# Performance work log

Measured on AMD Instinct MI355X. Metric: run time of the kernel, lower is better.

The kernel has to match this reference:

```python
import jax, jax.numpy as jnp
import numpy as np

EPS = 1e-5

def _fake_quant(w, axis):
    # symmetric int8 fake-quant with straight-through estimator
    s = jnp.max(jnp.abs(w), axis=axis, keepdims=True) / 127.0 + 1e-8
    q = jnp.clip(jnp.round(w / s), -127.0, 127.0) * s
    return w + jax.lax.stop_gradient(q - w)

def _qconv1x1(x, w, b):
    # x: [B, C_in, Q, H, W]; w: [C_out, C_in] (1x1 kernel); weight fake-quantized
    wq = _fake_quant(w, axis=1)
    return jnp.einsum('bcqhw,oc->boqhw', x, wq) + b[None, :, None, None, None]

def setup_inputs() -> dict:
    key = jax.random.key(0)
    ks = jax.random.split(key, 12)
    B, C, Q, H, W = 8, 256, 4, 40, 40
    x = jax.random.normal(ks[0], (B, C, Q, H, W), dtype=jnp.float32)
    scale = 1.0 / np.sqrt(C)
    Wq = jax.random.normal(ks[1], (C, C), dtype=jnp.float32) * scale
    Wk = jax.random.normal(ks[2], (C, C), dtype=jnp.float32) * scale
    Wv = jax.random.normal(ks[3], (C, C), dtype=jnp.float32) * scale
    Wp = jax.random.normal(ks[4], (C, C), dtype=jnp.float32) * scale
    bq = jnp.zeros((C,), jnp.float32)
    bk = jnp.zeros((C,), jnp.float32)
    bv = jnp.zeros((C,), jnp.float32)
    bp = jnp.zeros((C,), jnp.float32)
    gamma = jnp.ones((C,), jnp.float32)
    beta = jnp.zeros((C,), jnp.float32)
    return {"x": x, "Wq": Wq, "bq": bq, "Wk": Wk, "bk": bk,
            "Wv": Wv, "bv": bv, "Wp": Wp, "bp": bp,
            "gamma": gamma, "beta": beta}

def reference(x, Wq, bq, Wk, bk, Wv, bv, Wp, bp, gamma, beta):
    B, C, Q, H, W = x.shape
    q = _qconv1x1(x, Wq, bq)
    k = _qconv1x1(x, Wk, bk)
    v = _qconv1x1(x, Wv, bv)
    # per-rotation channel attention: [B, Q=4, C, H*W]
    qh = q.reshape(B, C, Q, H * W).transpose(0, 2, 1, 3)
    kh = k.reshape(B, C, Q, H * W).transpose(0, 2, 1, 3)
    vh = v.reshape(B, C, Q, H * W).transpose(0, 2, 1, 3)
    scale = 1.0 / jnp.sqrt(jnp.float32(C // 4))
    attn = jnp.einsum('bqcn,bqdn->bqcd', qh, kh) * scale  # [B,4,C,C]
    attn = jax.nn.softmax(attn, axis=-1)
    out = jnp.einsum('bqcd,bqdn->bqcn', attn, vh)  # [B,4,C,HW]
    out = out.transpose(0, 2, 1, 3).reshape(B, C, Q, H, W)
    out = _qconv1x1(out, Wp, bp)
    # IQBN: per-channel batchnorm with int8 fake-quantized gamma
    mean = jnp.mean(out, axis=(0, 2, 3, 4), keepdims=True)
    var = jnp.var(out, axis=(0, 2, 3, 4), keepdims=True)
    g = _fake_quant(gamma, axis=None)[None, :, None, None, None]
    b = beta[None, :, None, None, None]
    out = (out - mean) * jax.lax.rsqrt(var + EPS) * g + b
    return out
```

## Files before the change

kernel.cpp:

```cpp
#include <hip/hip_runtime.h>
#include <math.h>

#define BB 8
#define CCH 256
#define QQ 4
#define NN 1600
#define BQN 32
#define SP 51200
#define EPSF 1e-5f

typedef __attribute__((ext_vector_type(8))) short bf16x8;
typedef __attribute__((ext_vector_type(4))) float f32x4;

static __device__ inline ushort f2bf(float f) {
  union { float f; unsigned u; } v; v.f = f;
  return (ushort)((v.u + 0x7fffu + ((v.u >> 16) & 1u)) >> 16);
}
static __device__ inline float bf2f(ushort u) {
  union { unsigned u; float f; } v; v.u = ((unsigned)u) << 16;
  return v.f;
}
static __device__ inline void gld16(const ushort* g, ushort* l) {
  __builtin_amdgcn_global_load_lds(
      (const __attribute__((address_space(1))) unsigned int*)g,
      (__attribute__((address_space(3))) unsigned int*)l, 16, 0, 0);
}

__global__ void quant_weights_kernel(const float* Wq, const float* Wk,
                                     const float* Wv, const float* Wp,
                                     const float* gamma,
                                     ushort* wq, ushort* wk, ushort* wvT, ushort* wp,
                                     float* gq, float* r) {
  __shared__ float red[256];
  int blk = blockIdx.x;
  int tid = threadIdx.x;
  if (blk < 1024) {
    int mat = blk >> 8;
    int row = blk & 255;
    const float* W = (mat == 0) ? Wq : (mat == 1) ? Wk : (mat == 2) ? Wv : Wp;
    float w = W[row * 256 + tid];
    red[tid] = fabsf(w);
    __syncthreads();
    for (int s = 128; s > 0; s >>= 1) {
      if (tid < s) red[tid] = fmaxf(red[tid], red[tid + s]);
      __syncthreads();
    }
    float s = red[0] / 127.0f + 1e-8f;
    float q = fminf(fmaxf(rintf(w / s), -127.0f), 127.0f) * s;
    ushort qb = f2bf(q);
    if (mat == 0)      wq[row * 256 + tid] = qb;
    else if (mat == 1) wk[row * 256 + tid] = qb;
    else if (mat == 2) wvT[tid * 256 + row] = qb;
    else               wp[row * 256 + tid] = qb;
  } else {
    float g = gamma[tid];
    red[tid] = fabsf(g);
    __syncthreads();
    for (int s = 128; s > 0; s >>= 1) {
      if (tid < s) red[tid] = fmaxf(red[tid], red[tid + s]);
      __syncthreads();
    }
    float s = red[0] / 127.0f + 1e-8f;
    gq[tid] = fminf(fmaxf(rintf(g / s), -127.0f), 127.0f) * s;
    for (int i = tid; i < BQN * 256; i += 256) r[i] = 0.f;
  }
}

__global__ __launch_bounds__(256)
void prep_kernel(const float* __restrict__ x, ushort* __restrict__ xb,
                 ushort* __restrict__ xT, float* __restrict__ r) {
  int bqi = blockIdx.z, b = bqi >> 2, q = bqi & 3;
  int s0 = blockIdx.x * 64, c0 = blockIdx.y * 64;
  __shared__ ushort lT[64 * 66];
  int tid = threadIdx.x;
  int c = tid >> 2, nch = (tid & 3) * 16;
  const float* xp = x + ((size_t)(b * CCH + c0 + c) * QQ + q) * NN + s0 + nch;
  union { ushort u[16]; int4 v[2]; } nb;
  float s = 0.f;
#pragma unroll
  for (int j = 0; j < 4; j++) {
    float4 f = ((const float4*)xp)[j];
    s += f.x + f.y + f.z + f.w;
    nb.u[j * 4 + 0] = f2bf(f.x);
    nb.u[j * 4 + 1] = f2bf(f.y);
    nb.u[j * 4 + 2] = f2bf(f.z);
    nb.u[j * 4 + 3] = f2bf(f.w);
    lT[c * 66 + nch + j * 4 + 0] = nb.u[j * 4 + 0];
    lT[c * 66 + nch + j * 4 + 1] = nb.u[j * 4 + 1];
    lT[c * 66 + nch + j * 4 + 2] = nb.u[j * 4 + 2];
    lT[c * 66 + nch + j * 4 + 3] = nb.u[j * 4 + 3];
  }
  ushort* xbp = xb + (size_t)bqi * (CCH * NN) + (size_t)(c0 + c) * NN + s0 + nch;
  *(int4*)xbp = nb.v[0];
  *((int4*)xbp + 1) = nb.v[1];
  s += __shfl_down(s, 2);
  s += __shfl_down(s, 1);
  if ((tid & 3) == 0) atomicAdd(&r[bqi * 256 + c0 + c], s);
  __syncthreads();
  int n = tid >> 2, cch = (tid & 3) * 16;
  union { ushort u[16]; int4 v[2]; } o;
#pragma unroll
  for (int i = 0; i < 16; i++) o.u[i] = lT[(cch + i) * 66 + n];
  ushort* dst = xT + (size_t)(bqi * NN + s0 + n) * CCH + c0 + cch;
  *(int4*)dst = o.v[0];
  *((int4*)dst + 1) = o.v[1];
}

__global__ __launch_bounds__(256)
void gram_kernel(const ushort* __restrict__ xb, ushort* __restrict__ Gh,
                 ushort* __restrict__ Gl) {
  __shared__ __align__(16) char smem[32768];
  float* lC = (float*)smem;
  int z = blockIdx.z;
  int mBase = blockIdx.y * 128, nBase = blockIdx.x * 128;
  int tid = threadIdx.x, wave = tid >> 6, lane = tid & 63;
  int wm = wave >> 1, wn = wave & 1;
  int col = lane & 15, quad = lane >> 4;
  int srow = tid >> 2, skc = (tid & 3) * 8;
  const ushort* X = xb + (size_t)z * (CCH * NN);
  const ushort* gA  = X + (size_t)(mBase + srow) * NN + skc;
  const ushort* gA2 = gA + (size_t)64 * NN;
  const ushort* gB  = X + (size_t)(nBase + srow) * NN + skc;
  const ushort* gB2 = gB + (size_t)64 * NN;
  ushort* sA1[2]; ushort* sA2[2]; ushort* sB1[2]; ushort* sB2[2];
#pragma unroll
  for (int b = 0; b < 2; b++) {
    ushort* lAb = (ushort*)(smem + b * 16384);
    ushort* lBb = (ushort*)(smem + b * 16384 + 8192);
    sA1[b] = &lAb[srow * 32 + skc];
    sA2[b] = &lAb[(64 + srow) * 32 + skc];
    sB1[b] = &lBb[srow * 32 + skc];
    sB2[b] = &lBb[(64 + srow) * 32 + skc];
  }
  f32x4 acc[4][4];
#pragma unroll
  for (int i = 0; i < 4; i++)
#pragma unroll
    for (int j = 0; j < 4; j++) acc[i][j] = (f32x4){0.f, 0.f, 0.f, 0.f};

  const int nIter = NN / 32;
  gld16(gA, sA1[0]); gld16(gA2, sA2[0]); gld16(gB, sB1[0]); gld16(gB2, sB2[0]);
  for (int it = 0; it < nIter; ++it) {
    int cur = it & 1;
    __syncthreads();
    if (it + 1 < nIter) {
      int kt = (it + 1) << 5, nxt = cur ^ 1;
      gld16(gA + kt, sA1[nxt]); gld16(gA2 + kt, sA2[nxt]);
      gld16(gB + kt, sB1[nxt]); gld16(gB2 + kt, sB2[nxt]);
    }
    const ushort* lAc = (const ushort*)(smem + cur * 16384);
    const ushort* lBc = (const ushort*)(smem + cur * 16384 + 8192);
    bf16x8 af[4], bfr[4];
#pragma unroll
    for (int i = 0; i < 4; i++)
      af[i] = *(const bf16x8*)&lAc[(wm * 64 + i * 16 + col) * 32 + quad * 8];
#pragma unroll
    for (int j = 0; j < 4; j++)
      bfr[j] = *(const bf16x8*)&lBc[(wn * 64 + j * 16 + col) * 32 + quad * 8];
#pragma unroll
    for (int i = 0; i < 4; i++)
#pragma unroll
      for (int j = 0; j < 4; j++)
        acc[i][j] = __builtin_amdgcn_mfma_f32_16x16x32_bf16(af[i], bfr[j], acc[i][j], 0, 0, 0);
  }
  __syncthreads();
  float* lCw = lC + wave * 16 * 68;
  int mW = mBase + wm * 64, nW = nBase + wn * 64;
#pragma unroll
  for (int i = 0; i < 4; i++) {
#pragma unroll
    for (int j = 0; j < 4; j++)
#pragma unroll
      for (int rg = 0; rg < 4; rg++)
        lCw[(quad * 4 + rg) * 68 + j * 16 + col] = acc[i][j][rg];
    int mrow0 = mW + i * 16;
    int rr = lane & 15, cc = lane >> 4;
    union { ushort u[16]; int4 v[2]; } oh, ol;
#pragma unroll
    for (int t = 0; t < 16; t++) {
      float vfl = lCw[rr * 68 + cc * 16 + t];
      ushort hh = f2bf(vfl);
      oh.u[t] = hh;
      ol.u[t] = f2bf(vfl - bf2f(hh));
    }
    size_t off = (size_t)z * 65536 + (size_t)(mrow0 + rr) * 256 + nW + cc * 16;
    *(int4*)(Gh + off) = oh.v[0];
    *((int4*)(Gh + off) + 1) = oh.v[1];
    *(int4*)(Gl + off) = ol.v[0];
    *((int4*)(Gl + off) + 1) = ol.v[1];
  }
}

template<int MODE>
__global__ __launch_bounds__(256)
void gemm256(const ushort* __restrict__ A, long sA, const ushort* __restrict__ A2,
             const ushort* __restrict__ B, long sB, const ushort* __restrict__ B2,
             void* __restrict__ C1, void* __restrict__ C2, long sC) {
  __shared__ __align__(16) char smem[24576];
  ushort* lA = (ushort*)smem;
  ushort* lB = (ushort*)(smem + 8192);
  ushort* lX = (ushort*)(smem + 16384);
  float* lC = (float*)smem;
  int z = blockIdx.z;
  int mBase = blockIdx.y * 128, nBase = blockIdx.x * 128;
  int tid = threadIdx.x, wave = tid >> 6, lane = tid & 63;
  int wm = wave >> 1, wn = wave & 1;
  int col = lane & 15, quad = lane >> 4;
  int srow = tid >> 2, skc = (tid & 3) * 8;
  const ushort* Az = A + (size_t)z * sA;
  const ushort* Bz = B + (size_t)z * sB;
  const ushort* gA  = Az + (size_t)(mBase + srow) * 256 + skc;
  const ushort* gA2r = gA + 64 * 256;
  const ushort* gB  = Bz + (size_t)(nBase + srow) * 256 + skc;
  const ushort* gB2r = gB + 64 * 256;
  const ushort* gX = nullptr;
  const ushort* gX2 = nullptr;
  if (MODE == 0) {
    const ushort* Xz = B2 + (size_t)z * sB;
    gX = Xz + (size_t)(nBase + srow) * 256 + skc;
    gX2 = gX + 64 * 256;
  } else if (MODE == 1) {
    const ushort* Xz = A2 + (size_t)z * sA;
    gX = Xz + (size_t)(mBase + srow) * 256 + skc;
    gX2 = gX + 64 * 256;
  }
  ushort* dA1 = &lA[srow * 32 + skc]; ushort* dA2 = &lA[(64 + srow) * 32 + skc];
  ushort* dB1 = &lB[srow * 32 + skc]; ushort* dB2 = &lB[(64 + srow) * 32 + skc];
  ushort* dX1 = &lX[srow * 32 + skc]; ushort* dX2 = &lX[(64 + srow) * 32 + skc];

  f32x4 acc[4][4];
#pragma unroll
  for (int i = 0; i < 4; i++)
#pragma unroll
    for (int j = 0; j < 4; j++) acc[i][j] = (f32x4){0.f, 0.f, 0.f, 0.f};

  for (int kt = 0; kt < 256; kt += 32) {
    __syncthreads();
    gld16(gA + kt, dA1); gld16(gA2r + kt, dA2);
    gld16(gB + kt, dB1); gld16(gB2r + kt, dB2);
    if (MODE <= 1) { gld16(gX + kt, dX1); gld16(gX2 + kt, dX2); }
    __syncthreads();
    bf16x8 af[4], bfr[4], xf[4];
#pragma unroll
    for (int i = 0; i < 4; i++)
      af[i] = *(const bf16x8*)&lA[(wm * 64 + i * 16 + col) * 32 + quad * 8];
#pragma unroll
    for (int j = 0; j < 4; j++)
      bfr[j] = *(const bf16x8*)&lB[(wn * 64 + j * 16 + col) * 32 + quad * 8];
    if (MODE == 0) {
#pragma unroll
      for (int j = 0; j < 4; j++)
        xf[j] = *(const bf16x8*)&lX[(wn * 64 + j * 16 + col) * 32 + quad * 8];
    } else if (MODE == 1) {
#pragma unroll
      for (int i = 0; i < 4; i++)
        xf[i] = *(const bf16x8*)&lX[(wm * 64 + i * 16 + col) * 32 + quad * 8];
    }
#pragma unroll
    for (int i = 0; i < 4; i++)
#pragma unroll
      for (int j = 0; j < 4; j++) {
        acc[i][j] = __builtin_amdgcn_mfma_f32_16x16x32_bf16(af[i], bfr[j], acc[i][j], 0, 0, 0);
        if (MODE == 0)
          acc[i][j] = __builtin_amdgcn_mfma_f32_16x16x32_bf16(af[i], xf[j], acc[i][j], 0, 0, 0);
        else if (MODE == 1)
          acc[i][j] = __builtin_amdgcn_mfma_f32_16x16x32_bf16(xf[i], bfr[j], acc[i][j], 0, 0, 0);
      }
  }
  __syncthreads();
  float* lCw = lC + wave * 16 * 68;
  int mW = mBase + wm * 64, nW = nBase + wn * 64;
#pragma unroll
  for (int i = 0; i < 4; i++) {
#pragma unroll
    for (int j = 0; j < 4; j++)
#pragma unroll
      for (int rg = 0; rg < 4; rg++)
        lCw[(quad * 4 + rg) * 68 + j * 16 + col] = acc[i][j][rg];
    int mrow0 = mW + i * 16;
    int rr = lane & 15, cc = lane >> 4;
    if (MODE == 0) {
      union { ushort u[16]; int4 v[2]; } oh, ol;
#pragma unroll
      for (int t = 0; t < 16; t++) {
        float vfl = lCw[rr * 68 + cc * 16 + t];
        ushort hh = f2bf(vfl);
        oh.u[t] = hh;
        ol.u[t] = f2bf(vfl - bf2f(hh));
      }
      size_t off = (size_t)z * sC + (size_t)(mrow0 + rr) * 256 + nW + cc * 16;
      *(int4*)((ushort*)C1 + off) = oh.v[0];
      *((int4*)((ushort*)C1 + off) + 1) = oh.v[1];
      *(int4*)((ushort*)C2 + off) = ol.v[0];
      *((int4*)((ushort*)C2 + off) + 1) = ol.v[1];
    } else if (MODE == 1) {
      float* C = (float*)C1 + (size_t)z * sC + (size_t)(mrow0 + rr) * 256 + nW + cc * 16;
#pragma unroll
      for (int v = 0; v < 4; v++) {
        float4 f;
        f.x = lCw[rr * 68 + cc * 16 + v * 4 + 0];
        f.y = lCw[rr * 68 + cc * 16 + v * 4 + 1];
        f.z = lCw[rr * 68 + cc * 16 + v * 4 + 2];
        f.w = lCw[rr * 68 + cc * 16 + v * 4 + 3];
        *(float4*)(C + v * 4) = f;
      }
    } else if (MODE == 2) {
      int n = nW + lane;
      union { ushort u[16]; int4 v[2]; } o;
#pragma unroll
      for (int t = 0; t < 16; t++) o.u[t] = f2bf(lCw[t * 68 + lane]);
      ushort* C = (ushort*)C1 + (size_t)z * sC + (size_t)n * 256 + mrow0;
      *(int4*)C = o.v[0];
      *((int4*)C + 1) = o.v[1];
    } else {
      union { ushort u[16]; int4 v[2]; } o;
#pragma unroll
      for (int t = 0; t < 16; t++) o.u[t] = f2bf(lCw[rr * 68 + cc * 16 + t]);
      ushort* C = (ushort*)C1 + (size_t)z * sC + (size_t)(mrow0 + rr) * 256 + nW + cc * 16;
      *(int4*)C = o.v[0];
      *((int4*)C + 1) = o.v[1];
    }
  }
}

__global__ void uv_kernel(const ushort* __restrict__ wq, const ushort* __restrict__ wk,
                          const float* __restrict__ r, float* __restrict__ u,
                          float* __restrict__ vv) {
  int bq = blockIdx.x, sel = blockIdx.y, c = threadIdx.x;
  const ushort* W = sel ? wk : wq;
  float s = 0.f;
  for (int i = 0; i < 256; i++) s += bf2f(W[c * 256 + i]) * r[bq * 256 + i];
  (sel ? vv : u)[bq * 256 + c] = s;
}

__global__ void softmax_kernel(const float* __restrict__ S, const float* __restrict__ u,
                               const float* __restrict__ vv, const float* __restrict__ bqv,
                               const float* __restrict__ bkv, const float* __restrict__ bvv,
                               ushort* __restrict__ P, float* __restrict__ pb) {
  int bi = blockIdx.x;
  int bq = bi >> 8, rw = bi & 255;
  int tid = threadIdx.x;
  size_t off = (size_t)bq * 65536 + (size_t)rw * 256 + tid;
  float bqc = bqv[rw], bkd = bkv[tid];
  float val = 0.125f * (S[off] + u[bq * 256 + rw] * bkd + bqc * vv[bq * 256 + tid]
                        + 1600.0f * bqc * bkd);
  __shared__ float red[256];
  red[tid] = val;
  __syncthreads();
  for (int s = 128; s > 0; s >>= 1) {
    if (tid < s) red[tid] = fmaxf(red[tid], red[tid + s]);
    __syncthreads();
  }
  float m = red[0];
  __syncthreads();
  float e = expf(val - m);
  red[tid] = e;
  __syncthreads();
  for (int s = 128; s > 0; s >>= 1) {
    if (tid < s) red[tid] += red[tid + s];
    __syncthreads();
  }
  float p = e / red[0];
  P[off] = f2bf(p);
  __syncthreads();
  red[tid] = p * bvv[tid];
  __syncthreads();
  for (int s = 128; s > 0; s >>= 1) {
    if (tid < s) red[tid] += red[tid + s];
    __syncthreads();
  }
  if (tid == 0) pb[bq * 256 + rw] = red[0];
}

__global__ void bo_kernel(const ushort* __restrict__ wp, const float* __restrict__ pb,
                          const float* __restrict__ bp, float* __restrict__ bo) {
  int bq = blockIdx.x, o = threadIdx.x;
  float s = bp[o];
  for (int c = 0; c < 256; c++) s += bf2f(wp[o * 256 + c]) * pb[bq * 256 + c];
  bo[bq * 256 + o] = s;
}

__global__ __launch_bounds__(256)
void final_kernel(const ushort* __restrict__ Tm, const ushort* __restrict__ xT,
                  const float* __restrict__ bo, float* __restrict__ out,
                  float* __restrict__ part) {
  __shared__ __align__(16) char smem[32768];
  float* lC = (float*)smem;
  __shared__ float psS[2][128];
  __shared__ float psS2[2][128];
  int z = blockIdx.z;
  int mBase = blockIdx.y * 128, nBase = blockIdx.x * 128;
  int tid = threadIdx.x, wave = tid >> 6, lane = tid & 63;
  int wm = wave >> 1, wn = wave & 1;
  int col = lane & 15, quad = lane >> 4;
  int srow = tid >> 2, skc = (tid & 3) * 8;
  const ushort* Az = Tm + (size_t)z * 65536;
  const ushort* Bz = xT + (size_t)z * (NN * 256);
  const ushort* gA  = Az + (size_t)(mBase + srow) * 256 + skc;
  const ushort* gA2 = gA + 64 * 256;
  int br1 = nBase + srow;      br1 = br1 < NN ? br1 : NN - 1;
  int br2 = nBase + 64 + srow; br2 = br2 < NN ? br2 : NN - 1;
  const ushort* gB  = Bz + (size_t)br1 * 256 + skc;
  const ushort* gB2 = Bz + (size_t)br2 * 256 + skc;
  ushort* sA1[2]; ushort* sA2[2]; ushort* sB1[2]; ushort* sB2[2];
#pragma unroll
  for (int b = 0; b < 2; b++) {
    ushort* lAb = (ushort*)(smem + b * 16384);
    ushort* lBb = (ushort*)(smem + b * 16384 + 8192);
    sA1[b] = &lAb[srow * 32 + skc];
    sA2[b] = &lAb[(64 + srow) * 32 + skc];
    sB1[b] = &lBb[srow * 32 + skc];
    sB2[b] = &lBb[(64 + srow) * 32 + skc];
  }
  f32x4 acc[4][4];
#pragma unroll
  for (int i = 0; i < 4; i++)
#pragma unroll
    for (int j = 0; j < 4; j++) acc[i][j] = (f32x4){0.f, 0.f, 0.f, 0.f};

  const int nIter = 8;
  gld16(gA, sA1[0]); gld16(gA2, sA2[0]); gld16(gB, sB1[0]); gld16(gB2, sB2[0]);
  for (int it = 0; it < nIter; ++it) {
    int cur = it & 1;
    __syncthreads();
    if (it + 1 < nIter) {
      int kt = (it + 1) << 5, nxt = cur ^ 1;
      gld16(gA + kt, sA1[nxt]); gld16(gA2 + kt, sA2[nxt]);
      gld16(gB + kt, sB1[nxt]); gld16(gB2 + kt, sB2[nxt]);
    }
    const ushort* lAc = (const ushort*)(smem + cur * 16384);
    const ushort* lBc = (const ushort*)(smem + cur * 16384 + 8192);
    bf16x8 af[4], bfr[4];
#pragma unroll
    for (int i = 0; i < 4; i++)
      af[i] = *(const bf16x8*)&lAc[(wm * 64 + i * 16 + col) * 32 + quad * 8];
#pragma unroll
    for (int j = 0; j < 4; j++)
      bfr[j] = *(const bf16x8*)&lBc[(wn * 64 + j * 16 + col) * 32 + quad * 8];
#pragma unroll
    for (int i = 0; i < 4; i++)
#pragma unroll
      for (int j = 0; j < 4; j++)
        acc[i][j] = __builtin_amdgcn_mfma_f32_16x16x32_bf16(af[i], bfr[j], acc[i][j], 0, 0, 0);
  }
  __syncthreads();
  float* lCw = lC + wave * 16 * 68;
  int mW = mBase + wm * 64, nW = nBase + wn * 64;
  int b = z >> 2, q = z & 3;
#pragma unroll
  for (int i = 0; i < 4; i++) {
#pragma unroll
    for (int j = 0; j < 4; j++)
#pragma unroll
      for (int rg = 0; rg < 4; rg++)
        lCw[(quad * 4 + rg) * 68 + j * 16 + col] = acc[i][j][rg];
    int mrow0 = mW + i * 16;
    int rr = lane & 15, cc = lane >> 4;
    int n0 = nW + cc * 16;
    float bi = bo[(size_t)z * 256 + mrow0 + rr];
    float ls = 0.f, ls2 = 0.f;
    if (n0 < NN) {
      float* C = out + (size_t)b * (CCH * QQ * NN)
               + (size_t)(mrow0 + rr) * (QQ * NN) + (size_t)q * NN + n0;
#pragma unroll
      for (int v = 0; v < 4; v++) {
        float4 f;
        f.x = lCw[rr * 68 + cc * 16 + v * 4 + 0] + bi;
        f.y = lCw[rr * 68 + cc * 16 + v * 4 + 1] + bi;
        f.z = lCw[rr * 68 + cc * 16 + v * 4 + 2] + bi;
        f.w = lCw[rr * 68 + cc * 16 + v * 4 + 3] + bi;
        *(float4*)(C + v * 4) = f;
        ls  += f.x + f.y + f.z + f.w;
        ls2 += f.x * f.x + f.y * f.y + f.z * f.z + f.w * f.w;
      }
    }
    ls  += __shfl_down(ls, 32);  ls  += __shfl_down(ls, 16);
    ls2 += __shfl_down(ls2, 32); ls2 += __shfl_down(ls2, 16);
    if (lane < 16) {
      psS[wn][wm * 64 + i * 16 + lane] = ls;
      psS2[wn][wm * 64 + i * 16 + lane] = ls2;
    }
  }
  __syncthreads();
  if (tid < 128) {
    float s  = psS[0][tid] + psS[1][tid];
    float s2 = psS2[0][tid] + psS2[1][tid];
    int slot = z * 13 + blockIdx.x;
    part[(size_t)slot * 256 + mBase + tid] = s;
    part[416 * 256 + (size_t)slot * 256 + mBase + tid] = s2;
  }
}

__global__ void stats2_kernel(const float* __restrict__ part, float* __restrict__ st) {
  int o = blockIdx.x;
  int tid = threadIdx.x;
  float s = 0.f, s2 = 0.f;
  for (int x = tid; x < 416; x += 256) {
    s  += part[(size_t)x * 256 + o];
    s2 += part[416 * 256 + (size_t)x * 256 + o];
  }
  __shared__ float rs[256], rs2[256];
  rs[tid] = s; rs2[tid] = s2;
  __syncthreads();
  for (int t = 128; t > 0; t >>= 1) {
    if (tid < t) { rs[tid] += rs[tid + t]; rs2[tid] += rs2[tid + t]; }
    __syncthreads();
  }
  if (tid == 0) {
    float inv = 1.0f / (float)(BQN * NN);
    float mean = rs[0] * inv;
    float var = rs2[0] * inv - mean * mean;
    st[o] = mean;
    st[CCH + o] = var;
  }
}

__global__ __launch_bounds__(256)
void bn_kernel(float* __restrict__ out, const float* __restrict__ st,
               const float* __restrict__ gq, const float* __restrict__ beta) {
  size_t i4 = (size_t)blockIdx.x * 256 + threadIdx.x;
  int o = (int)((i4 / 1600) & 255);
  float mean = st[o];
  float g = rsqrtf(st[CCH + o] + EPSF) * gq[o];
  float be = beta[o];
  float4 f = ((const float4*)out)[i4];
  f.x = (f.x - mean) * g + be;
  f.y = (f.y - mean) * g + be;
  f.z = (f.z - mean) * g + be;
  f.w = (f.w - mean) * g + be;
  ((float4*)out)[i4] = f;
}

extern "C" void kernel_launch(void* const* d_in, const int* in_sizes, int n_in,
                              void* d_out, int out_size, void* d_ws, size_t ws_size,
                              hipStream_t stream) {
  const float* x     = (const float*)d_in[0];
  const float* Wq    = (const float*)d_in[1];
  const float* bq    = (const float*)d_in[2];
  const float* Wk    = (const float*)d_in[3];
  const float* bk    = (const float*)d_in[4];
  const float* Wv    = (const float*)d_in[5];
  const float* bv    = (const float*)d_in[6];
  const float* Wp    = (const float*)d_in[7];
  const float* bp    = (const float*)d_in[8];
  const float* gamma = (const float*)d_in[9];
  const float* beta  = (const float*)d_in[10];
  float* out = (float*)d_out;

  ushort* h    = (ushort*)d_ws;
  ushort* wq   = h;
  ushort* wk   = wq + 65536;
  ushort* wp   = wk + 65536;
  ushort* wvT  = wp + 65536;
  ushort* xb   = wvT + 65536;
  ushort* xT   = xb + (size_t)BQN * CCH * NN;
  ushort* Gh   = xT + (size_t)BQN * CCH * NN;
  ushort* Gl   = Gh + (size_t)BQN * 65536;
  ushort* M1h  = Gl + (size_t)BQN * 65536;
  ushort* M1l  = M1h + (size_t)BQN * 65536;
  ushort* P    = M1l + (size_t)BQN * 65536;
  ushort* N1t  = P + (size_t)BQN * 65536;
  ushort* Tm   = N1t + (size_t)BQN * 65536;
  float*  S    = (float*)(Tm + (size_t)BQN * 65536);
  float*  r    = S + (size_t)BQN * 65536;
  float*  u    = r + 8192;
  float*  vv   = u + 8192;
  float*  pb   = vv + 8192;
  float*  bo   = pb + 8192;
  float*  gq   = bo + 8192;
  float*  st   = gq + 256;
  float*  part = st + 512;

  quant_weights_kernel<<<1025, 256, 0, stream>>>(Wq, Wk, Wv, Wp, gamma,
                                                 wq, wk, wvT, wp, gq, r);
  prep_kernel<<<dim3(NN / 64, CCH / 64, BQN), 256, 0, stream>>>(x, xb, xT, r);
  uv_kernel<<<dim3(BQN, 2), 256, 0, stream>>>(wq, wk, r, u, vv);
  gram_kernel<<<dim3(2, 2, BQN), 256, 0, stream>>>(xb, Gh, Gl);
  gemm256<0><<<dim3(2, 2, BQN), 256, 0, stream>>>(
      wq, 0, nullptr, Gh, 65536, Gl, M1h, M1l, 65536);
  gemm256<1><<<dim3(2, 2, BQN), 256, 0, stream>>>(
      M1h, 65536, M1l, wk, 0, nullptr, S, nullptr, 65536);
  softmax_kernel<<<BQN * CCH, 256, 0, stream>>>(S, u, vv, bq, bk, bv, P, pb);
  gemm256<2><<<dim3(2, 2, BQN), 256, 0, stream>>>(
      P, 65536, nullptr, wvT, 0, nullptr, N1t, nullptr, 65536);
  gemm256<3><<<dim3(2, 2, BQN), 256, 0, stream>>>(
      wp, 0, nullptr, N1t, 65536, nullptr, Tm, nullptr, 65536);
  bo_kernel<<<BQN, 256, 0, stream>>>(wp, pb, bp, bo);
  final_kernel<<<dim3(13, 2, BQN), 256, 0, stream>>>(Tm, xT, bo, out, part);
  stats2_kernel<<<CCH, 256, 0, stream>>>(part, st);
  bn_kernel<<<(BB * CCH * QQ * NN / 4) / 256, 256, 0, stream>>>(out, st, gq, beta);
}
```

Before: 285.8 us.

## Compute BN stats analytically from Gram matrix, fuse BN into final, retile GEMMs

Computes the batchnorm mean and variance analytically from the Gram matrix, the composed projection Tm, and the row sums, using a new GEMM mode plus a bo_d1 kernel. The normalization then folds into final_kernel, which removes the separate stats pass and the read-modify-write pass over the 52 MB output. The small 256x256 GEMMs move from 128x128 to 64x64 tiles with double-buffered LDS loads to fill more CUs. Softmax switches to one wave per row with shuffle reductions, and uv/bo read transposed weights for coalescing. The variance is now E[x^2]-mean^2 assembled from bf16 operands and atomics, which risks precision loss.

```diff
diff --git a/kernel.cpp b/kernel.cpp
--- a/kernel.cpp
+++ b/kernel.cpp
@@ -30,7 +30,9 @@
                                      const float* Wv, const float* Wp,
                                      const float* gamma,
                                      ushort* wq, ushort* wk, ushort* wvT, ushort* wp,
-                                     float* gq, float* r) {
+                                     ushort* wqT, ushort* wkT, ushort* wpT,
+                                     float* gq, float* r, float* d2,
+                                     float* m_acc, float* v_acc) {
   __shared__ float red[256];
   int blk = blockIdx.x;
   int tid = threadIdx.x;
@@ -48,10 +50,10 @@
     float s = red[0] / 127.0f + 1e-8f;
     float q = fminf(fmaxf(rintf(w / s), -127.0f), 127.0f) * s;
     ushort qb = f2bf(q);
-    if (mat == 0)      wq[row * 256 + tid] = qb;
-    else if (mat == 1) wk[row * 256 + tid] = qb;
-    else if (mat == 2) wvT[tid * 256 + row] = qb;
-    else               wp[row * 256 + tid] = qb;
+    if (mat == 0)      { wq[row * 256 + tid] = qb; wqT[tid * 256 + row] = qb; }
+    else if (mat == 1) { wk[row * 256 + tid] = qb; wkT[tid * 256 + row] = qb; }
+    else if (mat == 2) { wvT[tid * 256 + row] = qb; }
+    else               { wp[row * 256 + tid] = qb; wpT[tid * 256 + row] = qb; }
   } else {
     float g = gamma[tid];
     red[tid] = fabsf(g);
@@ -62,7 +64,9 @@
     }
     float s = red[0] / 127.0f + 1e-8f;
     gq[tid] = fminf(fmaxf(rintf(g / s), -127.0f), 127.0f) * s;
-    for (int i = tid; i < BQN * 256; i += 256) r[i] = 0.f;
+    for (int i = tid; i < BQN * 256; i += 256) { r[i] = 0.f; d2[i] = 0.f; }
+    m_acc[tid] = 0.f;
+    v_acc[tid] = 0.f;
   }
 }
 
@@ -80,15 +84,16 @@
 #pragma unroll
   for (int j = 0; j < 4; j++) {
     float4 f = ((const float4*)xp)[j];
-    s += f.x + f.y + f.z + f.w;
-    nb.u[j * 4 + 0] = f2bf(f.x);
-    nb.u[j * 4 + 1] = f2bf(f.y);
-    nb.u[j * 4 + 2] = f2bf(f.z);
-    nb.u[j * 4 + 3] = f2bf(f.w);
-    lT[c * 66 + nch + j * 4 + 0] = nb.u[j * 4 + 0];
-    lT[c * 66 + nch + j * 4 + 1] = nb.u[j * 4 + 1];
-    lT[c * 66 + nch + j * 4 + 2] = nb.u[j * 4 + 2];
-    lT[c * 66 + nch + j * 4 + 3] = nb.u[j * 4 + 3];
+    ushort b0 = f2bf(f.x), b1 = f2bf(f.y), b2 = f2bf(f.z), b3 = f2bf(f.w);
+    s += bf2f(b0) + bf2f(b1) + bf2f(b2) + bf2f(b3);
+    nb.u[j * 4 + 0] = b0;
+    nb.u[j * 4 + 1] = b1;
+    nb.u[j * 4 + 2] = b2;
+    nb.u[j * 4 + 3] = b3;
+    lT[c * 66 + nch + j * 4 + 0] = b0;
+    lT[c * 66 + nch + j * 4 + 1] = b1;
+    lT[c * 66 + nch + j * 4 + 2] = b2;
+    lT[c * 66 + nch + j * 4 + 3] = b3;
   }
   ushort* xbp = xb + (size_t)bqi * (CCH * NN) + (size_t)(c0 + c) * NN + s0 + nch;
   *(int4*)xbp = nb.v[0];
@@ -193,201 +198,232 @@
 
 template<int MODE>
 __global__ __launch_bounds__(256)
-void gemm256(const ushort* __restrict__ A, long sA, const ushort* __restrict__ A2,
-             const ushort* __restrict__ B, long sB, const ushort* __restrict__ B2,
-             void* __restrict__ C1, void* __restrict__ C2, long sC) {
-  __shared__ __align__(16) char smem[24576];
-  ushort* lA = (ushort*)smem;
-  ushort* lB = (ushort*)(smem + 8192);
-  ushort* lX = (ushort*)(smem + 16384);
-  float* lC = (float*)smem;
+void gemm64(const ushort* __restrict__ A, long sA, const ushort* __restrict__ A2,
+            const ushort* __restrict__ B, long sB, const ushort* __restrict__ B2,
+            void* __restrict__ C1, void* __restrict__ C2, long sC) {
+  constexpr bool SPB = (MODE == 0 || MODE == 4);
+  constexpr bool SPA = (MODE == 1);
+  constexpr int BUFB = (SPA || SPB) ? 12288 : 8192;
+  __shared__ __align__(16) char smem[2 * BUFB];
   int z = blockIdx.z;
-  int mBase = blockIdx.y * 128, nBase = blockIdx.x * 128;
+  int mBase = blockIdx.y * 64, nBase = blockIdx.x * 64;
   int tid = threadIdx.x, wave = tid >> 6, lane = tid & 63;
   int wm = wave >> 1, wn = wave & 1;
   int col = lane & 15, quad = lane >> 4;
-  int srow = tid >> 2, skc = (tid & 3) * 8;
-  const ushort* Az = A + (size_t)z * sA;
-  const ushort* Bz = B + (size_t)z * sB;
-  const ushort* gA  = Az + (size_t)(mBase + srow) * 256 + skc;
-  const ushort* gA2r = gA + 64 * 256;
-  const ushort* gB  = Bz + (size_t)(nBase + srow) * 256 + skc;
-  const ushort* gB2r = gB + 64 * 256;
+  const ushort* gA = A + (size_t)z * sA + (size_t)(mBase + (tid >> 2)) * 256 + (tid & 3) * 8;
+  const ushort* gB = B + (size_t)z * sB + (size_t)(nBase + (tid >> 2)) * 256 + (tid & 3) * 8;
   const ushort* gX = nullptr;
-  const ushort* gX2 = nullptr;
-  if (MODE == 0) {
-    const ushort* Xz = B2 + (size_t)z * sB;
-    gX = Xz + (size_t)(nBase + srow) * 256 + skc;
-    gX2 = gX + 64 * 256;
-  } else if (MODE == 1) {
-    const ushort* Xz = A2 + (size_t)z * sA;
-    gX = Xz + (size_t)(mBase + srow) * 256 + skc;
-    gX2 = gX + 64 * 256;
-  }
-  ushort* dA1 = &lA[srow * 32 + skc]; ushort* dA2 = &lA[(64 + srow) * 32 + skc];
-  ushort* dB1 = &lB[srow * 32 + skc]; ushort* dB2 = &lB[(64 + srow) * 32 + skc];
-  ushort* dX1 = &lX[srow * 32 + skc]; ushort* dX2 = &lX[(64 + srow) * 32 + skc];
-
-  f32x4 acc[4][4];
-#pragma unroll
-  for (int i = 0; i < 4; i++)
-#pragma unroll
-    for (int j = 0; j < 4; j++) acc[i][j] = (f32x4){0.f, 0.f, 0.f, 0.f};
-
-  for (int kt = 0; kt < 256; kt += 32) {
+  if (SPB) gX = B2 + (size_t)z * sB + (size_t)(nBase + (tid >> 2)) * 256 + (tid & 3) * 8;
+  if (SPA) gX = A2 + (size_t)z * sA + (size_t)(mBase + (tid >> 2)) * 256 + (tid & 3) * 8;
+
+  f32x4 acc[2][2];
+#pragma unroll
+  for (int i = 0; i < 2; i++)
+#pragma unroll
+    for (int j = 0; j < 2; j++) acc[i][j] = (f32x4){0.f, 0.f, 0.f, 0.f};
+
+  {
+    char* bb = smem;
+    gld16(gA, (ushort*)bb + tid * 8);
+    gld16(gB, (ushort*)(bb + 4096) + tid * 8);
+    if (SPA || SPB) gld16(gX, (ushort*)(bb + 8192) + tid * 8);
+  }
+  for (int it = 0; it < 8; ++it) {
+    int cur = it & 1;
     __syncthreads();
-    gld16(gA + kt, dA1); gld16(gA2r + kt, dA2);
-    gld16(gB + kt, dB1); gld16(gB2r + kt, dB2);
-    if (MODE <= 1) { gld16(gX + kt, dX1); gld16(gX2 + kt, dX2); }
-    __syncthreads();
-    bf16x8 af[4], bfr[4], xf[4];
-#pragma unroll
-    for (int i = 0; i < 4; i++)
-      af[i] = *(const bf16x8*)&lA[(wm * 64 + i * 16 + col) * 32 + quad * 8];
-#pragma unroll
-    for (int j = 0; j < 4; j++)
-      bfr[j] = *(const bf16x8*)&lB[(wn * 64 + j * 16 + col) * 32 + quad * 8];
-    if (MODE == 0) {
-#pragma unroll
-      for (int j = 0; j < 4; j++)
-        xf[j] = *(const bf16x8*)&lX[(wn * 64 + j * 16 + col) * 32 + quad * 8];
-    } else if (MODE == 1) {
-#pragma unroll
-      for (int i = 0; i < 4; i++)
-        xf[i] = *(const bf16x8*)&lX[(wm * 64 + i * 16 + col) * 32 + quad * 8];
-    }
-#pragma unroll
-    for (int i = 0; i < 4; i++)
-#pragma unroll
-      for (int j = 0; j < 4; j++) {
-        acc[i][j] = __builtin_amdgcn_mfma_f32_16x16x32_bf16(af[i], bfr[j], acc[i][j], 0, 0, 0);
-        if (MODE == 0)
+    if (it + 1 < 8) {
+      int kt = (it + 1) * 32;
+      char* bb = smem + (cur ^ 1) * BUFB;
+      gld16(gA + kt, (ushort*)bb + tid * 8);
+      gld16(gB + kt, (ushort*)(bb + 4096) + tid * 8);
+      if (SPA || SPB) gld16(gX + kt, (ushort*)(bb + 8192) + tid * 8);
+    }
+    const ushort* lA = (const ushort*)(smem + cur * BUFB);
+    const ushort* lB = lA + 2048;
+    const ushort* lX = lA + 4096;
+    bf16x8 af[2], bfv[2], xf[2];
+#pragma unroll
+    for (int i = 0; i < 2; i++)
+      af[i] = *(const bf16x8*)&lA[(wm * 32 + i * 16 + col) * 32 + quad * 8];
+#pragma unroll
+    for (int j = 0; j < 2; j++)
+      bfv[j] = *(const bf16x8*)&lB[(wn * 32 + j * 16 + col) * 32 + quad * 8];
+    if (SPB) {
+#pragma unroll
+      for (int j = 0; j < 2; j++)
+        xf[j] = *(const bf16x8*)&lX[(wn * 32 + j * 16 + col) * 32 + quad * 8];
+    } else if (SPA) {
+#pragma unroll
+      for (int i = 0; i < 2; i++)
+        xf[i] = *(const bf16x8*)&lX[(wm * 32 + i * 16 + col) * 32 + quad * 8];
+    }
+#pragma unroll
+    for (int i = 0; i < 2; i++)
+#pragma unroll
+      for (int j = 0; j < 2; j++) {
+        acc[i][j] = __builtin_amdgcn_mfma_f32_16x16x32_bf16(af[i], bfv[j], acc[i][j], 0, 0, 0);
+        if (SPB)
           acc[i][j] = __builtin_amdgcn_mfma_f32_16x16x32_bf16(af[i], xf[j], acc[i][j], 0, 0, 0);
-        else if (MODE == 1)
-          acc[i][j] = __builtin_amdgcn_mfma_f32_16x16x32_bf16(xf[i], bfr[j], acc[i][j], 0, 0, 0);
+        if (SPA)
+          acc[i][j] = __builtin_amdgcn_mfma_f32_16x16x32_bf16(xf[i], bfv[j], acc[i][j], 0, 0, 0);
       }
   }
+
+  if (MODE == 4) {
+    const ushort* Tz = A + (size_t)z * sA;
+    float* d2 = (float*)C1;
+#pragma unroll
+    for (int i = 0; i < 2; i++) {
+      int mr = mBase + wm * 32 + i * 16 + quad * 4;
+#pragma unroll
+      for (int rg = 0; rg < 4; rg++) {
+        float p = 0.f;
+#pragma unroll
+        for (int j = 0; j < 2; j++)
+          p += acc[i][j][rg] * bf2f(Tz[(mr + rg) * 256 + nBase + wn * 32 + j * 16 + col]);
+        p += __shfl_down(p, 8);
+        p += __shfl_down(p, 4);
+        p += __shfl_down(p, 2);
+        p += __shfl_down(p, 1);
+        if (col == 0) atomicAdd(d2 + z * 256 + mr + rg, p);
+      }
+    }
+    return;
+  }
+
   __syncthreads();
-  float* lCw = lC + wave * 16 * 68;
-  int mW = mBase + wm * 64, nW = nBase + wn * 64;
-#pragma unroll
-  for (int i = 0; i < 4; i++) {
-#pragma unroll
-    for (int j = 0; j < 4; j++)
+  float* lCw = (float*)smem + wave * (16 * 36);
+#pragma unroll
+  for (int i = 0; i < 2; i++) {
+#pragma unroll
+    for (int j = 0; j < 2; j++)
 #pragma unroll
       for (int rg = 0; rg < 4; rg++)
-        lCw[(quad * 4 + rg) * 68 + j * 16 + col] = acc[i][j][rg];
-    int mrow0 = mW + i * 16;
-    int rr = lane & 15, cc = lane >> 4;
-    if (MODE == 0) {
-      union { ushort u[16]; int4 v[2]; } oh, ol;
-#pragma unroll
-      for (int t = 0; t < 16; t++) {
-        float vfl = lCw[rr * 68 + cc * 16 + t];
-        ushort hh = f2bf(vfl);
+        lCw[(quad * 4 + rg) * 36 + j * 16 + col] = acc[i][j][rg];
+    int mrow0 = mBase + wm * 32 + i * 16;
+    int nW = nBase + wn * 32;
+    if (MODE == 1) {
+      int rr = lane >> 2, cc = (lane & 3) * 8;
+      float* C = (float*)C1 + (size_t)z * sC + (size_t)(mrow0 + rr) * 256 + nW + cc;
+      float4 f0, f1;
+      f0.x = lCw[rr * 36 + cc + 0]; f0.y = lCw[rr * 36 + cc + 1];
+      f0.z = lCw[rr * 36 + cc + 2]; f0.w = lCw[rr * 36 + cc + 3];
+      f1.x = lCw[rr * 36 + cc + 4]; f1.y = lCw[rr * 36 + cc + 5];
+      f1.z = lCw[rr * 36 + cc + 6]; f1.w = lCw[rr * 36 + cc + 7];
+      *(float4*)C = f0;
+      *(float4*)(C + 4) = f1;
+    } else if (MODE == 0) {
+      int rr = lane >> 2, cc = (lane & 3) * 8;
+      union { ushort u[8]; int4 v; } oh, ol;
+#pragma unroll
+      for (int t = 0; t < 8; t++) {
+        float vf = lCw[rr * 36 + cc + t];
+        ushort hh = f2bf(vf);
         oh.u[t] = hh;
-        ol.u[t] = f2bf(vfl - bf2f(hh));
+        ol.u[t] = f2bf(vf - bf2f(hh));
       }
-      size_t off = (size_t)z * sC + (size_t)(mrow0 + rr) * 256 + nW + cc * 16;
-      *(int4*)((ushort*)C1 + off) = oh.v[0];
-      *((int4*)((ushort*)C1 + off) + 1) = oh.v[1];
-      *(int4*)((ushort*)C2 + off) = ol.v[0];
-      *((int4*)((ushort*)C2 + off) + 1) = ol.v[1];
-    } else if (MODE == 1) {
-      float* C = (float*)C1 + (size_t)z * sC + (size_t)(mrow0 + rr) * 256 + nW + cc * 16;
-#pragma unroll
-      for (int v = 0; v < 4; v++) {
-        float4 f;
-        f.x = lCw[rr * 68 + cc * 16 + v * 4 + 0];
-        f.y = lCw[rr * 68 + cc * 16 + v * 4 + 1];
-        f.z = lCw[rr * 68 + cc * 16 + v * 4 + 2];
-        f.w = lCw[rr * 68 + cc * 16 + v * 4 + 3];
-        *(float4*)(C + v * 4) = f;
+      size_t off = (size_t)z * sC + (size_t)(mrow0 + rr) * 256 + nW + cc;
+      *(int4*)((ushort*)C1 + off) = oh.v;
+      *(int4*)((ushort*)C2 + off) = ol.v;
+    } else {
+      if (MODE == 3) {
+        int rr = lane >> 2, cc = (lane & 3) * 8;
+        union { ushort u[8]; int4 v; } o;
+#pragma unroll
+        for (int t = 0; t < 8; t++) o.u[t] = f2bf(lCw[rr * 36 + cc + t]);
+        *(int4*)((ushort*)C1 + (size_t)z * sC + (size_t)(mrow0 + rr) * 256 + nW + cc) = o.v;
       }
-    } else if (MODE == 2) {
-      int n = nW + lane;
-      union { ushort u[16]; int4 v[2]; } o;
-#pragma unroll
-      for (int t = 0; t < 16; t++) o.u[t] = f2bf(lCw[t * 68 + lane]);
-      ushort* C = (ushort*)C1 + (size_t)z * sC + (size_t)n * 256 + mrow0;
-      *(int4*)C = o.v[0];
-      *((int4*)C + 1) = o.v[1];
-    } else {
-      union { ushort u[16]; int4 v[2]; } o;
-#pragma unroll
-      for (int t = 0; t < 16; t++) o.u[t] = f2bf(lCw[rr * 68 + cc * 16 + t]);
-      ushort* C = (ushort*)C1 + (size_t)z * sC + (size_t)(mrow0 + rr) * 256 + nW + cc * 16;
-      *(int4*)C = o.v[0];
-      *((int4*)C + 1) = o.v[1];
-    }
-  }
-}
-
-__global__ void uv_kernel(const ushort* __restrict__ wq, const ushort* __restrict__ wk,
-                          const float* __restrict__ r, float* __restrict__ u,
-                          float* __restrict__ vv) {
+      int nn = lane >> 1, mh = (lane & 1) * 8;
+      union { ushort u[8]; int4 v; } o2;
+#pragma unroll
+      for (int t = 0; t < 8; t++) o2.u[t] = f2bf(lCw[(mh + t) * 36 + nn]);
+      ushort* CT = (ushort*)((MODE == 2) ? C1 : C2);
+      *(int4*)(CT + (size_t)z * sC + (size_t)(nW + nn) * 256 + mrow0 + mh) = o2.v;
+    }
+  }
+}
+
+__global__ __launch_bounds__(256)
+void uv_kernel(const ushort* __restrict__ wqT, const ushort* __restrict__ wkT,
+               const float* __restrict__ r, float* __restrict__ u,
+               float* __restrict__ vv) {
   int bq = blockIdx.x, sel = blockIdx.y, c = threadIdx.x;
-  const ushort* W = sel ? wk : wq;
+  __shared__ float rs[256];
+  rs[c] = r[bq * 256 + c];
+  __syncthreads();
+  const ushort* WT = sel ? wkT : wqT;
   float s = 0.f;
-  for (int i = 0; i < 256; i++) s += bf2f(W[c * 256 + i]) * r[bq * 256 + i];
+  for (int i = 0; i < 256; i++) s += bf2f(WT[i * 256 + c]) * rs[i];
   (sel ? vv : u)[bq * 256 + c] = s;
 }
 
-__global__ void softmax_kernel(const float* __restrict__ S, const float* __restrict__ u,
-                               const float* __restrict__ vv, const float* __restrict__ bqv,
-                               const float* __restrict__ bkv, const float* __restrict__ bvv,
-                               ushort* __restrict__ P, float* __restrict__ pb) {
-  int bi = blockIdx.x;
-  int bq = bi >> 8, rw = bi & 255;
-  int tid = threadIdx.x;
-  size_t off = (size_t)bq * 65536 + (size_t)rw * 256 + tid;
-  float bqc = bqv[rw], bkd = bkv[tid];
-  float val = 0.125f * (S[off] + u[bq * 256 + rw] * bkd + bqc * vv[bq * 256 + tid]
-                        + 1600.0f * bqc * bkd);
-  __shared__ float red[256];
-  red[tid] = val;
+__global__ __launch_bounds__(256)
+void softmax_kernel(const float* __restrict__ S, const float* __restrict__ u,
+                    const float* __restrict__ vv, const float* __restrict__ bqv,
+                    const float* __restrict__ bkv, const float* __restrict__ bvv,
+                    ushort* __restrict__ P, float* __restrict__ pb) {
+  int wave = threadIdx.x >> 6, lane = threadIdx.x & 63;
+  int rglob = blockIdx.x * 4 + wave;
+  int bq = rglob >> 8, rw = rglob & 255;
+  size_t off = (size_t)rglob * 256;
+  int c0 = lane * 4;
+  float4 s4 = *(const float4*)(S + off + c0);
+  float4 v4 = *(const float4*)(vv + bq * 256 + c0);
+  float4 bk4 = *(const float4*)(bkv + c0);
+  float4 bv4 = *(const float4*)(bvv + c0);
+  float uu = u[bq * 256 + rw];
+  float bqc = bqv[rw];
+  float x0 = 0.125f * (s4.x + uu * bk4.x + bqc * v4.x + 1600.0f * bqc * bk4.x);
+  float x1 = 0.125f * (s4.y + uu * bk4.y + bqc * v4.y + 1600.0f * bqc * bk4.y);
+  float x2 = 0.125f * (s4.z + uu * bk4.z + bqc * v4.z + 1600.0f * bqc * bk4.z);
+  float x3 = 0.125f * (s4.w + uu * bk4.w + bqc * v4.w + 1600.0f * bqc * bk4.w);
+  float m = fmaxf(fmaxf(x0, x1), fmaxf(x2, x3));
+#pragma unroll
+  for (int s = 32; s > 0; s >>= 1) m = fmaxf(m, __shfl_xor(m, s));
+  float e0 = expf(x0 - m), e1 = expf(x1 - m), e2 = expf(x2 - m), e3 = expf(x3 - m);
+  float t = e0 + e1 + e2 + e3;
+#pragma unroll
+  for (int s = 32; s > 0; s >>= 1) t += __shfl_xor(t, s);
+  float is = 1.0f / t;
+  float p0 = e0 * is, p1 = e1 * is, p2 = e2 * is, p3 = e3 * is;
+  union { ushort u[4]; uint2 v; } o;
+  o.u[0] = f2bf(p0); o.u[1] = f2bf(p1); o.u[2] = f2bf(p2); o.u[3] = f2bf(p3);
+  *(uint2*)(P + off + c0) = o.v;
+  float d = p0 * bv4.x + p1 * bv4.y + p2 * bv4.z + p3 * bv4.w;
+#pragma unroll
+  for (int s = 32; s > 0; s >>= 1) d += __shfl_xor(d, s);
+  if (lane == 0) pb[rglob] = d;
+}
+
+__global__ __launch_bounds__(256)
+void bo_d1_kernel(const ushort* __restrict__ wpT, const ushort* __restrict__ TmT,
+                  const float* __restrict__ pb, const float* __restrict__ rb,
+                  const float* __restrict__ bp, const float* __restrict__ d2,
+                  float* __restrict__ bo, float* __restrict__ m_acc,
+                  float* __restrict__ v_acc) {
+  int z = blockIdx.x, o = threadIdx.x;
+  __shared__ float sp[256], sr[256];
+  sp[o] = pb[z * 256 + o];
+  sr[o] = rb[z * 256 + o];
   __syncthreads();
-  for (int s = 128; s > 0; s >>= 1) {
-    if (tid < s) red[tid] = fmaxf(red[tid], red[tid + s]);
-    __syncthreads();
-  }
-  float m = red[0];
-  __syncthreads();
-  float e = expf(val - m);
-  red[tid] = e;
-  __syncthreads();
-  for (int s = 128; s > 0; s >>= 1) {
-    if (tid < s) red[tid] += red[tid + s];
-    __syncthreads();
-  }
-  float p = e / red[0];
-  P[off] = f2bf(p);
-  __syncthreads();
-  red[tid] = p * bvv[tid];
-  __syncthreads();
-  for (int s = 128; s > 0; s >>= 1) {
-    if (tid < s) red[tid] += red[tid + s];
-    __syncthreads();
-  }
-  if (tid == 0) pb[bq * 256 + rw] = red[0];
-}
-
-__global__ void bo_kernel(const ushort* __restrict__ wp, const float* __restrict__ pb,
-                          const float* __restrict__ bp, float* __restrict__ bo) {
-  int bq = blockIdx.x, o = threadIdx.x;
-  float s = bp[o];
-  for (int c = 0; c < 256; c++) s += bf2f(wp[o * 256 + c]) * pb[bq * 256 + c];
-  bo[bq * 256 + o] = s;
+  float bv = bp[o], d1 = 0.f;
+  const ushort* Tz = TmT + (size_t)z * 65536;
+  for (int c = 0; c < 256; c++) {
+    bv += bf2f(wpT[c * 256 + o]) * sp[c];
+    d1 += bf2f(Tz[c * 256 + o]) * sr[c];
+  }
+  bo[z * 256 + o] = bv;
+  atomicAdd(m_acc + o, d1 + 1600.0f * bv);
+  atomicAdd(v_acc + o, d2[z * 256 + o] + 2.0f * bv * d1 + 1600.0f * bv * bv);
 }
 
 __global__ __launch_bounds__(256)
 void final_kernel(const ushort* __restrict__ Tm, const ushort* __restrict__ xT,
-                  const float* __restrict__ bo, float* __restrict__ out,
-                  float* __restrict__ part) {
+                  const float* __restrict__ bo, const float* __restrict__ m_acc,
+                  const float* __restrict__ v_acc, const float* __restrict__ gq,
+                  const float* __restrict__ beta, float* __restrict__ out) {
   __shared__ __align__(16) char smem[32768];
   float* lC = (float*)smem;
-  __shared__ float psS[2][128];
-  __shared__ float psS2[2][128];
   int z = blockIdx.z;
   int mBase = blockIdx.y * 128, nBase = blockIdx.x * 128;
   int tid = threadIdx.x, wave = tid >> 6, lane = tid & 63;
@@ -447,6 +483,7 @@
   float* lCw = lC + wave * 16 * 68;
   int mW = mBase + wm * 64, nW = nBase + wn * 64;
   int b = z >> 2, q = z & 3;
+  const float inv = 1.0f / (float)SP;
 #pragma unroll
   for (int i = 0; i < 4; i++) {
 #pragma unroll
@@ -457,78 +494,26 @@
     int mrow0 = mW + i * 16;
     int rr = lane & 15, cc = lane >> 4;
     int n0 = nW + cc * 16;
-    float bi = bo[(size_t)z * 256 + mrow0 + rr];
-    float ls = 0.f, ls2 = 0.f;
+    int o = mrow0 + rr;
+    float bi = bo[(size_t)z * 256 + o];
+    float mean = m_acc[o] * inv;
+    float var = v_acc[o] * inv - mean * mean;
+    float scl = rsqrtf(var + EPSF) * gq[o];
+    float be = beta[o];
     if (n0 < NN) {
       float* C = out + (size_t)b * (CCH * QQ * NN)
-               + (size_t)(mrow0 + rr) * (QQ * NN) + (size_t)q * NN + n0;
+               + (size_t)o * (QQ * NN) + (size_t)q * NN + n0;
 #pragma unroll
       for (int v = 0; v < 4; v++) {
         float4 f;
-        f.x = lCw[rr * 68 + cc * 16 + v * 4 + 0] + bi;
-        f.y = lCw[rr * 68 + cc * 16 + v * 4 + 1] + bi;
-        f.z = lCw[rr * 68 + cc * 16 + v * 4 + 2] + bi;
-        f.w = lCw[rr * 68 + cc * 16 + v * 4 + 3] + bi;
+        f.x = (lCw[rr * 68 + cc * 16 + v * 4 + 0] + bi - mean) * scl + be;
+        f.y = (lCw[rr * 68 + cc * 16 + v * 4 + 1] + bi - mean) * scl + be;
+        f.z = (lCw[rr * 68 + cc * 16 + v * 4 + 2] + bi - mean) * scl + be;
+        f.w = (lCw[rr * 68 + cc * 16 + v * 4 + 3] + bi - mean) * scl + be;
         *(float4*)(C + v * 4) = f;
-        ls  += f.x + f.y + f.z + f.w;
-        ls2 += f.x * f.x + f.y * f.y + f.z * f.z + f.w * f.w;
       }
     }
-    ls  += __shfl_down(ls, 32);  ls  += __shfl_down(ls, 16);
-    ls2 += __shfl_down(ls2, 32); ls2 += __shfl_down(ls2, 16);
-    if (lane < 16) {
-      psS[wn][wm * 64 + i * 16 + lane] = ls;
-      psS2[wn][wm * 64 + i * 16 + lane] = ls2;
-    }
-  }
-  __syncthreads();
-  if (tid < 128) {
-    float s  = psS[0][tid] + psS[1][tid];
-    float s2 = psS2[0][tid] + psS2[1][tid];
-    int slot = z * 13 + blockIdx.x;
-    part[(size_t)slot * 256 + mBase + tid] = s;
-    part[416 * 256 + (size_t)slot * 256 + mBase + tid] = s2;
-  }
-}
-
-__global__ void stats2_kernel(const float* __restrict__ part, float* __restrict__ st) {
-  int o = blockIdx.x;
-  int tid = threadIdx.x;
-  float s = 0.f, s2 = 0.f;
-  for (int x = tid; x < 416; x += 256) {
-    s  += part[(size_t)x * 256 + o];
-    s2 += part[416 * 256 + (size_t)x * 256 + o];
-  }
-  __shared__ float rs[256], rs2[256];
-  rs[tid] = s; rs2[tid] = s2;
-  __syncthreads();
-  for (int t = 128; t > 0; t >>= 1) {
-    if (tid < t) { rs[tid] += rs[tid + t]; rs2[tid] += rs2[tid + t]; }
-    __syncthreads();
-  }
-  if (tid == 0) {
-    float inv = 1.0f / (float)(BQN * NN);
-    float mean = rs[0] * inv;
-    float var = rs2[0] * inv - mean * mean;
-    st[o] = mean;
-    st[CCH + o] = var;
-  }
-}
-
-__global__ __launch_bounds__(256)
-void bn_kernel(float* __restrict__ out, const float* __restrict__ st,
-               const float* __restrict__ gq, const float* __restrict__ beta) {
-  size_t i4 = (size_t)blockIdx.x * 256 + threadIdx.x;
-  int o = (int)((i4 / 1600) & 255);
-  float mean = st[o];
-  float g = rsqrtf(st[CCH + o] + EPSF) * gq[o];
-  float be = beta[o];
-  float4 f = ((const float4*)out)[i4];
-  f.x = (f.x - mean) * g + be;
-  f.y = (f.y - mean) * g + be;
-  f.z = (f.z - mean) * g + be;
-  f.w = (f.w - mean) * g + be;
-  ((float4*)out)[i4] = f;
+  }
 }
 
 extern "C" void kernel_launch(void* const* d_in, const int* in_sizes, int n_in,
@@ -552,7 +537,10 @@
   ushort* wk   = wq + 65536;
   ushort* wp   = wk + 65536;
   ushort* wvT  = wp + 65536;
-  ushort* xb   = wvT + 65536;
+  ushort* wqT  = wvT + 65536;
+  ushort* wkT  = wqT + 65536;
+  ushort* wpT  = wkT + 65536;
+  ushort* xb   = wpT + 65536;
   ushort* xT   = xb + (size_t)BQN * CCH * NN;
   ushort* Gh   = xT + (size_t)BQN * CCH * NN;
   ushort* Gl   = Gh + (size_t)BQN * 65536;
@@ -561,32 +549,36 @@
   ushort* P    = M1l + (size_t)BQN * 65536;
   ushort* N1t  = P + (size_t)BQN * 65536;
   ushort* Tm   = N1t + (size_t)BQN * 65536;
-  float*  S    = (float*)(Tm + (size_t)BQN * 65536);
+  ushort* TmT  = Tm + (size_t)BQN * 65536;
+  float*  S    = (float*)(TmT + (size_t)BQN * 65536);
   float*  r    = S + (size_t)BQN * 65536;
   float*  u    = r + 8192;
   float*  vv   = u + 8192;
   float*  pb   = vv + 8192;
   float*  bo   = pb + 8192;
-  float*  gq   = bo + 8192;
-  float*  st   = gq + 256;
-  float*  part = st + 512;
+  float*  d2   = bo + 8192;
+  float*  m_acc = d2 + 8192;
+  float*  v_acc = m_acc + 256;
+  float*  gq   = v_acc + 256;
 
   quant_weights_kernel<<<1025, 256, 0, stream>>>(Wq, Wk, Wv, Wp, gamma,
-                                                 wq, wk, wvT, wp, gq, r);
+                                                 wq, wk, wvT, wp, wqT, wkT, wpT,
+                                                 gq, r, d2, m_acc, v_acc);
   prep_kernel<<<dim3(NN / 64, CCH / 64, BQN), 256, 0, stream>>>(x, xb, xT, r);
-  uv_kernel<<<dim3(BQN, 2), 256, 0, stream>>>(wq, wk, r, u, vv);
+  uv_kernel<<<dim3(BQN, 2), 256, 0, stream>>>(wqT, wkT, r, u, vv);
   gram_kernel<<<dim3(2, 2, BQN), 256, 0, stream>>>(xb, Gh, Gl);
-  gemm256<0><<<dim3(2, 2, BQN), 256, 0, stream>>>(
+  gemm64<0><<<dim3(4, 4, BQN), 256, 0, stream>>>(
       wq, 0, nullptr, Gh, 65536, Gl, M1h, M1l, 65536);
-  gemm256<1><<<dim3(2, 2, BQN), 256, 0, stream>>>(
+  gemm64<1><<<dim3(4, 4, BQN), 256, 0, stream>>>(
       M1h, 65536, M1l, wk, 0, nullptr, S, nullptr, 65536);
-  softmax_kernel<<<BQN * CCH, 256, 0, stream>>>(S, u, vv, bq, bk, bv, P, pb);
-  gemm256<2><<<dim3(2, 2, BQN), 256, 0, stream>>>(
+  softmax_kernel<<<BQN * CCH / 4, 256, 0, stream>>>(S, u, vv, bq, bk, bv, P, pb);
+  gemm64<2><<<dim3(4, 4, BQN), 256, 0, stream>>>(
       P, 65536, nullptr, wvT, 0, nullptr, N1t, nullptr, 65536);
-  gemm256<3><<<dim3(2, 2, BQN), 256, 0, stream>>>(
-      wp, 0, nullptr, N1t, 65536, nullptr, Tm, nullptr, 65536);
-  bo_kernel<<<BQN, 256, 0, stream>>>(wp, pb, bp, bo);
-  final_kernel<<<dim3(13, 2, BQN), 256, 0, stream>>>(Tm, xT, bo, out, part);
-  stats2_kernel<<<CCH, 256, 0, stream>>>(part, st);
-  bn_kernel<<<(BB * CCH * QQ * NN / 4) / 256, 256, 0, stream>>>(out, st, gq, beta);
-}
+  gemm64<3><<<dim3(4, 4, BQN), 256, 0, stream>>>(
+      wp, 0, nullptr, N1t, 65536, nullptr, Tm, TmT, 65536);
+  gemm64<4><<<dim3(4, 4, BQN), 256, 0, stream>>>(
+      Tm, 65536, nullptr, Gh, 65536, Gl, d2, nullptr, 0);
+  bo_d1_kernel<<<BQN, 256, 0, stream>>>(wpT, TmT, pb, r, bp, d2, bo, m_acc, v_acc);
+  final_kernel<<<dim3(13, 2, BQN), 256, 0, stream>>>(Tm, xT, bo, m_acc, v_acc,
+                                                     gq, beta, out);
+}
```

After: 264.4 us. 1.08x faster.
